# Kernel tuning notes

Measured on AMD Instinct MI355X. Metric: run time of the kernel, lower is better.

Reference implementation:

```python
import jax, jax.numpy as jnp
import numpy as np

INPUT_SIZE = 1
HIDDEN_SIZE = 50
OUTPUT_SIZE = 1
BATCH = 16384
SEQ_LEN = 2048


def setup_inputs() -> dict:
    key = jax.random.key(0)
    ks = jax.random.split(key, 8)
    s_ih = 1.0 / np.sqrt(HIDDEN_SIZE)
    x = jax.random.normal(ks[0], (BATCH, SEQ_LEN, INPUT_SIZE), dtype=jnp.float32)
    # PyTorch nn.LSTM params: weight_ih_l0 [4H, I], weight_hh_l0 [4H, H], biases [4H]
    w_ih = jax.random.uniform(ks[1], (4 * HIDDEN_SIZE, INPUT_SIZE), jnp.float32, -s_ih, s_ih)
    w_hh = jax.random.uniform(ks[2], (4 * HIDDEN_SIZE, HIDDEN_SIZE), jnp.float32, -s_ih, s_ih)
    b_ih = jax.random.uniform(ks[3], (4 * HIDDEN_SIZE,), jnp.float32, -s_ih, s_ih)
    b_hh = jax.random.uniform(ks[4], (4 * HIDDEN_SIZE,), jnp.float32, -s_ih, s_ih)
    # fc head: Linear(hidden_size, output_size)
    w_fc = jax.random.uniform(ks[5], (OUTPUT_SIZE, HIDDEN_SIZE), jnp.float32, -s_ih, s_ih)
    b_fc = jax.random.uniform(ks[6], (OUTPUT_SIZE,), jnp.float32, -s_ih, s_ih)
    return {"x": x, "w_ih": w_ih, "w_hh": w_hh, "b_ih": b_ih, "b_hh": b_hh,
            "w_fc": w_fc, "b_fc": b_fc}


def reference(x, w_ih, w_hh, b_ih, b_hh, w_fc, b_fc):
    B = x.shape[0]
    H = w_hh.shape[1]
    xT = jnp.swapaxes(x, 0, 1)                      # [T, B, I]
    # precompute input contribution to gates for all timesteps: [T, B, 4H]
    x_proj = jnp.einsum('tbi,gi->tbg', xT, w_ih) + b_ih + b_hh

    def step(carry, xp):
        h, c = carry
        gates = xp + h @ w_hh.T                     # [B, 4H]
        i, f, g, o = jnp.split(gates, 4, axis=-1)   # PyTorch gate order: i, f, g, o
        i = jax.nn.sigmoid(i)
        f = jax.nn.sigmoid(f)
        g = jnp.tanh(g)
        o = jax.nn.sigmoid(o)
        c = f * c + i * g
        h = o * jnp.tanh(c)
        return (h, c), None

    h0 = jnp.zeros((B, H), x.dtype)
    (h_last, _), _ = jax.lax.scan(step, (h0, h0), x_proj)
    # fc applied to last timestep's hidden state
    return h_last @ w_fc.T + b_fc                   # [B, 1]
```

## Files before the change

kernel.cpp:

```cpp
#include <hip/hip_runtime.h>
#include <cstdint>

typedef __attribute__((ext_vector_type(8))) short short8;
typedef __attribute__((ext_vector_type(4))) float f32x4;
typedef __attribute__((ext_vector_type(2))) float f32x2;

#define TPB  256
#define MB   16
#define HS   50
#define HSTR 72
#define XSTR 68
#define L2E  1.4426950408889634f
#define L2E2 2.8853900817779268f

__device__ __forceinline__ float ex2(float x) {
#if __has_builtin(__builtin_amdgcn_exp2f)
  return __builtin_amdgcn_exp2f(x);
#else
  float r; asm("v_exp_f32 %0, %1" : "=v"(r) : "v"(x)); return r;
#endif
}
__device__ __forceinline__ float rcp_(float x) {
#if __has_builtin(__builtin_amdgcn_rcpf)
  return __builtin_amdgcn_rcpf(x);
#else
  float r; asm("v_rcp_f32 %0, %1" : "=v"(r) : "v"(x)); return r;
#endif
}
__device__ __forceinline__ unsigned short bf16_rne(float f) {
  unsigned r;
  asm("v_cvt_pk_bf16_f32 %0, %1, %2" : "=v"(r) : "v"(f), "v"(f));
  return (unsigned short)r;
}
__device__ __forceinline__ float bf16f(unsigned short h) {
  union { unsigned u; float f; } v; v.u = ((unsigned)h) << 16; return v.f;
}
__device__ __forceinline__ unsigned packx(float f) {
  unsigned short hi = bf16_rne(f);
  unsigned short lo = bf16_rne(f - bf16f(hi));
  return (unsigned)hi | ((unsigned)lo << 16);
}
__device__ __forceinline__ int swcol(int row, int col) {
  return (((col >> 3) ^ ((row >> 2) & 3)) << 3) | (col & 7);
}

__global__ __launch_bounds__(TPB, 4)
void lstm_mfma5(const float* __restrict__ x,
                const float* __restrict__ w_ih,
                const float* __restrict__ w_hh,
                const float* __restrict__ b_ih,
                const float* __restrict__ b_hh,
                const float* __restrict__ w_fc,
                const float* __restrict__ b_fc,
                float* __restrict__ out, int T)
{
  __shared__ __attribute__((aligned(16))) unsigned short hbuf[2][MB][HSTR];
  __shared__ __attribute__((aligned(16))) unsigned x_lds[2][MB][XSTR];

  switch ((blockIdx.x >> 8) & 3) {
    case 1: __builtin_amdgcn_s_sleep(3); break;
    case 2: __builtin_amdgcn_s_sleep(6); break;
    case 3: __builtin_amdgcn_s_sleep(9); break;
    default: break;
  }

  const int tid  = threadIdx.x;
  const int wid  = tid >> 6;
  const int lane = tid & 63;
  const int l15  = lane & 15;
  const int lhi  = lane >> 4;
  const int b0   = blockIdx.x * MB;
  const int j    = wid * 16 + l15;
  const bool jval = (j < HS);
  const bool inj  = (lhi == 2);

  short8 Bh[4][2], Bl0[4];
  #pragma unroll
  for (int s = 0; s < 4; ++s) {
    const float sc = (s == 2) ? L2E2 : L2E;
    float wsc = 0.f, bsc = 0.f;
    if (jval) {
      int row = s * HS + j;
      wsc = w_ih[row] * sc;
      bsc = (b_ih[row] + b_hh[row]) * sc;
    }
    const unsigned short wh = bf16_rne(wsc);
    const unsigned short wl = bf16_rne(wsc - bf16f(wh));
    const unsigned short bh = bf16_rne(bsc);
    const unsigned short bl = bf16_rne(bsc - bf16f(bh));
    #pragma unroll
    for (int i = 0; i < 8; ++i) {
      int k = lhi * 8 + i;
      float val = jval ? w_hh[(s * HS + j) * HS + k] * sc : 0.f;
      unsigned short hi = bf16_rne(val);
      Bh[s][0][i] = (short)hi;
      Bl0[s][i]   = (short)bf16_rne(val - bf16f(hi));
    }
    #pragma unroll
    for (int i = 0; i < 8; ++i) {
      int k = 32 + lhi * 8 + i;
      unsigned short hv = 0;
      if (jval) {
        if (k < HS)                hv = bf16_rne(w_hh[(s * HS + j) * HS + k] * sc);
        else if (k == 50 || k == 51) hv = wh;
        else if (k == 52)          hv = wl;
        else if (k == 53)          hv = bh;
        else if (k == 54)          hv = bl;
      }
      Bh[s][1][i] = (short)hv;
    }
  }

  for (int idx = tid; idx < 2 * MB * HSTR; idx += TPB)
    (&hbuf[0][0][0])[idx] = 0;
  {
    int bb = tid >> 4, tt = (tid & 15) * 4;
    const f32x4 v = *(const f32x4*)(x + (size_t)(b0 + bb) * T + tt);
    uint4 up;
    up.x = packx(v[0]); up.y = packx(v[1]); up.z = packx(v[2]); up.w = packx(v[3]);
    *(uint4*)&x_lds[0][bb][tt] = up;
  }
  __syncthreads();

  const int keyr  = (l15 >> 2) & 3;
  const int offA0 = l15 * HSTR + ((lhi ^ keyr) << 3);
  const int offA1 = l15 * HSTR + (((lhi + 4) ^ keyr) << 3);
  const int offW0 = (lhi * 4) * HSTR + swcol(lhi * 4, j);

  f32x2 cA = {0.f, 0.f}, cB = {0.f, 0.f};
  f32x4 xf = {0.f, 0.f, 0.f, 0.f};

  const unsigned short* hr = &hbuf[0][0][0];
  unsigned short*       hw = &hbuf[1][0][0];
  const int nch = T >> 6;

  for (int t = 0; t < T; ++t) {
    if ((t & 63) == 16) {
      int c1 = (t >> 6) + 1;
      if (c1 < nch)
        xf = *(const f32x4*)(x + (size_t)(b0 + (tid >> 4)) * T + c1 * 64 + (tid & 15) * 4);
    }
    if ((t & 63) == 44) {
      int c1 = (t >> 6) + 1;
      if (c1 < nch) {
        uint4 up;
        up.x = packx(xf[0]); up.y = packx(xf[1]);
        up.z = packx(xf[2]); up.w = packx(xf[3]);
        *(uint4*)&x_lds[c1 & 1][tid >> 4][(tid & 15) * 4] = up;
      }
    }

    const unsigned xp = x_lds[(t >> 6) & 1][l15][t & 63];
    const short8 A0 = *(const short8*)(hr + offA0);
    union { short8 s8; unsigned u[4]; } a1;
    a1.s8 = *(const short8*)(hr + offA1);
    a1.u[1] = inj ? xp : a1.u[1];
    a1.u[2] = inj ? ((xp & 0xFFFFu) | 0x3F800000u) : a1.u[2];
    a1.u[3] = inj ? 0x00003F80u : a1.u[3];

    __builtin_amdgcn_s_setprio(1);
    f32x4 acc[4];
    #pragma unroll
    for (int s = 0; s < 4; ++s) {
      acc[s] = __builtin_amdgcn_mfma_f32_16x16x32_bf16(A0, Bh[s][0],
                   (f32x4){0.f, 0.f, 0.f, 0.f}, 0, 0, 0);
      acc[s] = __builtin_amdgcn_mfma_f32_16x16x32_bf16(A0, Bl0[s], acc[s], 0, 0, 0);
      acc[s] = __builtin_amdgcn_mfma_f32_16x16x32_bf16(a1.s8, Bh[s][1], acc[s], 0, 0, 0);
    }
    __builtin_amdgcn_s_setprio(0);

    f32x2 h2[2];
    #pragma unroll
    for (int P = 0; P < 2; ++P) {
      f32x2& c2 = P ? cB : cA;
      f32x2 u, v, w, z, q, rD, r3, vm1;
      u[0] = ex2(-acc[0][2*P]);  u[1] = ex2(-acc[0][2*P+1]);
      v[0] = ex2( acc[2][2*P]);  v[1] = ex2( acc[2][2*P+1]);
      w[0] = ex2(-acc[1][2*P]);  w[1] = ex2(-acc[1][2*P+1]);
      z[0] = ex2(-acc[3][2*P]);  z[1] = ex2(-acc[3][2*P+1]);
      f32x2 t1 = (u + 1.f) * (v + 1.f);
      f32x2 wp = w + 1.f;
      f32x2 D  = t1 * wp;
      rD[0] = rcp_(D[0]); rD[1] = rcp_(D[1]);
      vm1[0] = fmaf(v[0], L2E2, -L2E2);
      vm1[1] = fmaf(v[1], L2E2, -L2E2);
      f32x2 num = c2 * t1 + vm1 * wp;
      f32x2 cn = num * rD;
      cn[0] = fminf(fmaxf(cn[0], -86.f), 86.f);
      cn[1] = fminf(fmaxf(cn[1], -86.f), 86.f);
      c2 = cn;
      q[0] = ex2(cn[0]); q[1] = ex2(cn[1]);
      f32x2 t3 = (z + 1.f) * (q + 1.f);
      r3[0] = rcp_(t3[0]); r3[1] = rcp_(t3[1]);
      h2[P] = (q - 1.f) * r3;
    }

    if (jval) {
      hw[offW0           ] = bf16_rne(h2[0][0]);
      hw[offW0 +     HSTR] = bf16_rne(h2[0][1]);
      hw[offW0 + 2 * HSTR] = bf16_rne(h2[1][0]);
      hw[offW0 + 3 * HSTR] = bf16_rne(h2[1][1]);
    }

    __syncthreads();

    unsigned short* tmp = (unsigned short*)hr; hr = hw; hw = tmp;
  }

  if (tid < MB) {
    const unsigned short* hfin = hr + tid * HSTR;
    float s = 0.f;
    for (int jj = 0; jj < HS; ++jj)
      s = fmaf(bf16f(hfin[swcol(tid, jj)]), w_fc[jj], s);
    out[b0 + tid] = s + b_fc[0];
  }
}

extern "C" void kernel_launch(void* const* d_in, const int* in_sizes, int n_in,
                              void* d_out, int out_size, void* d_ws, size_t ws_size,
                              hipStream_t stream) {
  const float* x    = (const float*)d_in[0];
  const float* w_ih = (const float*)d_in[1];
  const float* w_hh = (const float*)d_in[2];
  const float* b_ih = (const float*)d_in[3];
  const float* b_hh = (const float*)d_in[4];
  const float* w_fc = (const float*)d_in[5];
  const float* b_fc = (const float*)d_in[6];
  float* out = (float*)d_out;

  const int B = out_size;
  const int T = in_sizes[0] / B;

  dim3 grid(B / MB), block(TPB);
  hipLaunchKernelGGL(lstm_mfma5, grid, block, 0, stream,
                     x, w_ih, w_hh, b_ih, b_hh, w_fc, b_fc, out, T);
}
```

Baseline: 2.283 ms.

## Drop low-bf16 weight MFMA, transpose MFMA operands, pack h stores, unroll by two

```diff
diff --git a/kernel.cpp b/kernel.cpp
--- a/kernel.cpp
+++ b/kernel.cpp
@@ -32,6 +32,11 @@
   asm("v_cvt_pk_bf16_f32 %0, %1, %2" : "=v"(r) : "v"(f), "v"(f));
   return (unsigned short)r;
 }
+__device__ __forceinline__ unsigned cvtpk2(float a, float b) {
+  unsigned r;
+  asm("v_cvt_pk_bf16_f32 %0, %1, %2" : "=v"(r) : "v"(a), "v"(b));
+  return r;
+}
 __device__ __forceinline__ float bf16f(unsigned short h) {
   union { unsigned u; float f; } v; v.u = ((unsigned)h) << 16; return v.f;
 }
@@ -45,7 +50,7 @@
 }
 
 __global__ __launch_bounds__(TPB, 4)
-void lstm_mfma5(const float* __restrict__ x,
+void lstm_mfma7(const float* __restrict__ x,
                 const float* __restrict__ w_ih,
                 const float* __restrict__ w_hh,
                 const float* __restrict__ b_ih,
@@ -57,13 +62,6 @@
   __shared__ __attribute__((aligned(16))) unsigned short hbuf[2][MB][HSTR];
   __shared__ __attribute__((aligned(16))) unsigned x_lds[2][MB][XSTR];
 
-  switch ((blockIdx.x >> 8) & 3) {
-    case 1: __builtin_amdgcn_s_sleep(3); break;
-    case 2: __builtin_amdgcn_s_sleep(6); break;
-    case 3: __builtin_amdgcn_s_sleep(9); break;
-    default: break;
-  }
-
   const int tid  = threadIdx.x;
   const int wid  = tid >> 6;
   const int lane = tid & 63;
@@ -74,7 +72,7 @@
   const bool jval = (j < HS);
   const bool inj  = (lhi == 2);
 
-  short8 Bh[4][2], Bl0[4];
+  short8 Wh[4][2];
   #pragma unroll
   for (int s = 0; s < 4; ++s) {
     const float sc = (s == 2) ? L2E2 : L2E;
@@ -91,23 +89,20 @@
     #pragma unroll
     for (int i = 0; i < 8; ++i) {
       int k = lhi * 8 + i;
-      float val = jval ? w_hh[(s * HS + j) * HS + k] * sc : 0.f;
-      unsigned short hi = bf16_rne(val);
-      Bh[s][0][i] = (short)hi;
-      Bl0[s][i]   = (short)bf16_rne(val - bf16f(hi));
+      Wh[s][0][i] = (short)(jval ? bf16_rne(w_hh[(s * HS + j) * HS + k] * sc) : 0);
     }
     #pragma unroll
     for (int i = 0; i < 8; ++i) {
       int k = 32 + lhi * 8 + i;
       unsigned short hv = 0;
       if (jval) {
-        if (k < HS)                hv = bf16_rne(w_hh[(s * HS + j) * HS + k] * sc);
+        if (k < HS)                  hv = bf16_rne(w_hh[(s * HS + j) * HS + k] * sc);
         else if (k == 50 || k == 51) hv = wh;
-        else if (k == 52)          hv = wl;
-        else if (k == 53)          hv = bh;
-        else if (k == 54)          hv = bl;
+        else if (k == 52)            hv = wl;
+        else if (k == 53)            hv = bh;
+        else if (k == 54)            hv = bl;
       }
-      Bh[s][1][i] = (short)hv;
+      Wh[s][1][i] = (short)hv;
     }
   }
 
@@ -125,16 +120,13 @@
   const int keyr  = (l15 >> 2) & 3;
   const int offA0 = l15 * HSTR + ((lhi ^ keyr) << 3);
   const int offA1 = l15 * HSTR + (((lhi + 4) ^ keyr) << 3);
-  const int offW0 = (lhi * 4) * HSTR + swcol(lhi * 4, j);
+  const int offW  = l15 * HSTR + ((((wid * 2 + (lhi >> 1)) ^ keyr) << 3)) + (lhi & 1) * 4;
 
   f32x2 cA = {0.f, 0.f}, cB = {0.f, 0.f};
   f32x4 xf = {0.f, 0.f, 0.f, 0.f};
-
-  const unsigned short* hr = &hbuf[0][0][0];
-  unsigned short*       hw = &hbuf[1][0][0];
   const int nch = T >> 6;
 
-  for (int t = 0; t < T; ++t) {
+  auto STEP = [&](const unsigned short* hr, unsigned short* hw, int t) {
     if ((t & 63) == 16) {
       int c1 = (t >> 6) + 1;
       if (c1 < nch)
@@ -151,64 +143,86 @@
     }
 
     const unsigned xp = x_lds[(t >> 6) & 1][l15][t & 63];
-    const short8 A0 = *(const short8*)(hr + offA0);
-    union { short8 s8; unsigned u[4]; } a1;
-    a1.s8 = *(const short8*)(hr + offA1);
-    a1.u[1] = inj ? xp : a1.u[1];
-    a1.u[2] = inj ? ((xp & 0xFFFFu) | 0x3F800000u) : a1.u[2];
-    a1.u[3] = inj ? 0x00003F80u : a1.u[3];
+    const short8 B0 = *(const short8*)(hr + offA0);
+    union { short8 s8; unsigned u[4]; } b1;
+    b1.s8 = *(const short8*)(hr + offA1);
+    b1.u[1] = inj ? xp : b1.u[1];
+    b1.u[2] = inj ? ((xp & 0xFFFFu) | 0x3F800000u) : b1.u[2];
+    b1.u[3] = inj ? 0x00003F80u : b1.u[3];
 
     __builtin_amdgcn_s_setprio(1);
     f32x4 acc[4];
     #pragma unroll
     for (int s = 0; s < 4; ++s) {
-      acc[s] = __builtin_amdgcn_mfma_f32_16x16x32_bf16(A0, Bh[s][0],
+      acc[s] = __builtin_amdgcn_mfma_f32_16x16x32_bf16(Wh[s][0], B0,
                    (f32x4){0.f, 0.f, 0.f, 0.f}, 0, 0, 0);
-      acc[s] = __builtin_amdgcn_mfma_f32_16x16x32_bf16(A0, Bl0[s], acc[s], 0, 0, 0);
-      acc[s] = __builtin_amdgcn_mfma_f32_16x16x32_bf16(a1.s8, Bh[s][1], acc[s], 0, 0, 0);
+      acc[s] = __builtin_amdgcn_mfma_f32_16x16x32_bf16(Wh[s][1], b1.s8, acc[s], 0, 0, 0);
     }
     __builtin_amdgcn_s_setprio(0);
 
-    f32x2 h2[2];
-    #pragma unroll
-    for (int P = 0; P < 2; ++P) {
-      f32x2& c2 = P ? cB : cA;
+    f32x2 h2A, h2B;
+    {
       f32x2 u, v, w, z, q, rD, r3, vm1;
-      u[0] = ex2(-acc[0][2*P]);  u[1] = ex2(-acc[0][2*P+1]);
-      v[0] = ex2( acc[2][2*P]);  v[1] = ex2( acc[2][2*P+1]);
-      w[0] = ex2(-acc[1][2*P]);  w[1] = ex2(-acc[1][2*P+1]);
-      z[0] = ex2(-acc[3][2*P]);  z[1] = ex2(-acc[3][2*P+1]);
+      u[0] = ex2(-acc[0][0]); u[1] = ex2(-acc[0][1]);
+      v[0] = ex2( acc[2][0]); v[1] = ex2( acc[2][1]);
+      w[0] = ex2(-acc[1][0]); w[1] = ex2(-acc[1][1]);
+      z[0] = ex2(-acc[3][0]); z[1] = ex2(-acc[3][1]);
       f32x2 t1 = (u + 1.f) * (v + 1.f);
       f32x2 wp = w + 1.f;
       f32x2 D  = t1 * wp;
       rD[0] = rcp_(D[0]); rD[1] = rcp_(D[1]);
       vm1[0] = fmaf(v[0], L2E2, -L2E2);
       vm1[1] = fmaf(v[1], L2E2, -L2E2);
-      f32x2 num = c2 * t1 + vm1 * wp;
+      f32x2 num = cA * t1 + vm1 * wp;
       f32x2 cn = num * rD;
       cn[0] = fminf(fmaxf(cn[0], -86.f), 86.f);
       cn[1] = fminf(fmaxf(cn[1], -86.f), 86.f);
-      c2 = cn;
+      cA = cn;
       q[0] = ex2(cn[0]); q[1] = ex2(cn[1]);
       f32x2 t3 = (z + 1.f) * (q + 1.f);
       r3[0] = rcp_(t3[0]); r3[1] = rcp_(t3[1]);
-      h2[P] = (q - 1.f) * r3;
-    }
-
-    if (jval) {
-      hw[offW0           ] = bf16_rne(h2[0][0]);
-      hw[offW0 +     HSTR] = bf16_rne(h2[0][1]);
-      hw[offW0 + 2 * HSTR] = bf16_rne(h2[1][0]);
-      hw[offW0 + 3 * HSTR] = bf16_rne(h2[1][1]);
-    }
+      h2A = (q - 1.f) * r3;
+    }
+    {
+      f32x2 u, v, w, z, q, rD, r3, vm1;
+      u[0] = ex2(-acc[0][2]); u[1] = ex2(-acc[0][3]);
+      v[0] = ex2( acc[2][2]); v[1] = ex2( acc[2][3]);
+      w[0] = ex2(-acc[1][2]); w[1] = ex2(-acc[1][3]);
+      z[0] = ex2(-acc[3][2]); z[1] = ex2(-acc[3][3]);
+      f32x2 t1 = (u + 1.f) * (v + 1.f);
+      f32x2 wp = w + 1.f;
+      f32x2 D  = t1 * wp;
+      rD[0] = rcp_(D[0]); rD[1] = rcp_(D[1]);
+      vm1[0] = fmaf(v[0], L2E2, -L2E2);
+      vm1[1] = fmaf(v[1], L2E2, -L2E2);
+      f32x2 num = cB * t1 + vm1 * wp;
+      f32x2 cn = num * rD;
+      cn[0] = fminf(fmaxf(cn[0], -86.f), 86.f);
+      cn[1] = fminf(fmaxf(cn[1], -86.f), 86.f);
+      cB = cn;
+      q[0] = ex2(cn[0]); q[1] = ex2(cn[1]);
+      f32x2 t3 = (z + 1.f) * (q + 1.f);
+      r3[0] = rcp_(t3[0]); r3[1] = rcp_(t3[1]);
+      h2B = (q - 1.f) * r3;
+    }
+
+    uint2 hwv;
+    hwv.x = cvtpk2(h2A[0], h2A[1]);
+    hwv.y = cvtpk2(h2B[0], h2B[1]);
+    *(uint2*)(hw + offW) = hwv;
 
     __syncthreads();
-
-    unsigned short* tmp = (unsigned short*)hr; hr = hw; hw = tmp;
+  };
+
+  unsigned short* hb0 = &hbuf[0][0][0];
+  unsigned short* hb1 = &hbuf[1][0][0];
+  for (int tb = 0; tb < T; tb += 2) {
+    STEP(hb0, hb1, tb);
+    STEP(hb1, hb0, tb + 1);
   }
 
   if (tid < MB) {
-    const unsigned short* hfin = hr + tid * HSTR;
+    const unsigned short* hfin = hb0 + tid * HSTR;
     float s = 0.f;
     for (int jj = 0; jj < HS; ++jj)
       s = fmaf(bf16f(hfin[swcol(tid, jj)]), w_fc[jj], s);
@@ -232,6 +246,6 @@
   const int T = in_sizes[0] / B;
 
   dim3 grid(B / MB), block(TPB);
-  hipLaunchKernelGGL(lstm_mfma5, grid, block, 0, stream,
+  hipLaunchKernelGGL(lstm_mfma7, grid, block, 0, stream,
                      x, w_ih, w_hh, b_ih, b_hh, w_fc, b_fc, out, T);
 }
```

New measurement: 1.963 ms. 1.16x faster.
